# Optimization experiments

Hardware: AMD Instinct MI355X
Metric: run time of the kernel (lower is better)

## Reference

```python
import jax, jax.numpy as jnp
import numpy as np

B, T, D, U, O = 256, 1024, 256, 512, 256

def setup_inputs() -> dict:
    key = jax.random.key(0)
    kx, kk, kr, kd = jax.random.split(key, 4)
    # he_normal-style scaling for weights
    x = jax.random.normal(kx, (B, T, D), dtype=jnp.float32)
    Wk = jax.random.normal(kk, (D, U), dtype=jnp.float32) * np.sqrt(2.0 / D)
    Wr = jax.random.normal(kr, (U, U), dtype=jnp.float32) * np.sqrt(2.0 / U)
    Wd = jax.random.normal(kd, (U, O), dtype=jnp.float32) * np.sqrt(2.0 / U)
    h0 = jnp.zeros((B, U), dtype=jnp.float32)  # stateful RNN initial state
    return {"x": x, "Wk": Wk, "Wr": Wr, "Wd": Wd, "h0": h0}

def reference(x, Wk, Wr, Wd, h0):
    # SimpleRNN (no bias): h_t = tanh(x_t @ Wk + h_{t-1} @ Wr)
    # return_sequences=False -> only final hidden state; then Dense (no bias).
    # Precompute the input projection for all timesteps in one big GEMM.
    xp = jnp.einsum('btd,du->btu', x, Wk)           # [B, T, U]
    xs = jnp.swapaxes(xp, 0, 1)                     # [T, B, U] for scan

    def step(h, xt):
        h = jnp.tanh(xt + h @ Wr)
        return h, None

    hT, _ = jax.lax.scan(step, h0, xs)              # hT: [B, U]
    return hT @ Wd                                  # [B, O]
```

## Files before the change

kernel.cpp:

```cpp
#include <hip/hip_runtime.h>
#include <hip/hip_bf16.h>

#define T_STEPS 1024
#define B_SZ 256
#define D_SZ 256
#define U_SZ 512
#define O_SZ 256
#define K_TOT 768

#define ROWS_PER_WG 16
#define COLS_PER_WG 32
#define GROUPS 16
#define COLGRPS 16
#define WAVES_PER_GROUP 32
#define WT_PITCH 776
#define CTR_PITCH 1056

typedef __attribute__((ext_vector_type(8))) short short8;
typedef __attribute__((ext_vector_type(4))) float floatx4;
typedef __attribute__((ext_vector_type(4))) int int4v;
typedef __attribute__((ext_vector_type(4))) unsigned int uint4v;

__device__ __forceinline__ unsigned short f2bf(float f) {
  union { float f; unsigned int u; } v; v.f = f;
  unsigned int r = v.u + 0x7FFFu + ((v.u >> 16) & 1u);
  return (unsigned short)(r >> 16);
}
__device__ __forceinline__ float bf2f(unsigned short s) {
  union { unsigned int u; float f; } v; v.u = ((unsigned int)s) << 16;
  return v.f;
}
__device__ __forceinline__ unsigned int pk2(float a, float b) {
  union { __hip_bfloat162 h; unsigned int u; } cv;
  cv.h = __float22bfloat162_rn(make_float2(a, b));
  return cv.u;
}

__device__ __forceinline__ void store_short_l3(const unsigned short* p, unsigned int v) {
  asm volatile("global_store_short %0, %1, off sc0 sc1"
               :: "v"(p), "v"(v) : "memory");
}
__device__ __forceinline__ int4v load16_l3(const unsigned short* p) {
  int4v r;
  asm volatile("global_load_dwordx4 %0, %1, off sc0 sc1"
               : "=v"(r) : "v"(p) : "memory");
  return r;
}
__device__ __forceinline__ void wait_vm0() {
  asm volatile("s_waitcnt vmcnt(0)" ::: "memory");
}
__device__ __forceinline__ unsigned int load_ctr_l3(const unsigned int* p) {
  unsigned int r;
  asm volatile("global_load_dword %0, %1, off sc0 sc1\n\ts_waitcnt vmcnt(0)"
               : "=v"(r) : "v"(p) : "memory");
  return r;
}

extern "C" __global__ void __launch_bounds__(128)
rnn_persistent(const float* __restrict__ x, const float* __restrict__ Wk,
               const float* __restrict__ Wr, const float* __restrict__ h0,
               unsigned short* __restrict__ Hbuf0, unsigned short* __restrict__ Hbuf1,
               unsigned int* __restrict__ ctr)
{
  __shared__ unsigned short Wt[COLS_PER_WG][WT_PITCH];

  const int bid  = blockIdx.x;
  const int g    = (bid & 7) + ((bid >> 7) << 3);
  const int c    = (bid >> 3) & 15;
  const int row0 = g * ROWS_PER_WG;
  const int col0 = c * COLS_PER_WG;
  const int tid  = threadIdx.x;
  const int wave = tid >> 6;
  const int lane = tid & 63;
  const int m    = lane & 15;
  const int quad = lane >> 4;
  unsigned int* gctr = ctr + g * CTR_PITCH;

  for (int idx = tid; idx < COLS_PER_WG * K_TOT; idx += 128) {
    int k  = idx >> 5;
    int cl = idx & 31;
    float w = (k < D_SZ) ? Wk[(size_t)k * U_SZ + col0 + cl]
                         : Wr[(size_t)(k - D_SZ) * U_SZ + col0 + cl];
    Wt[cl][k] = f2bf(w);
  }

  {
    int e  = tid * 4;
    int rr = e >> 5;
    int cl = e & 31;
    const float* src = h0 + (size_t)(row0 + rr) * U_SZ + col0 + cl;
    const unsigned short* dst = Hbuf0 + (size_t)(row0 + rr) * U_SZ + col0 + cl;
    store_short_l3(dst + 0, f2bf(src[0]));
    store_short_l3(dst + 1, f2bf(src[1]));
    store_short_l3(dst + 2, f2bf(src[2]));
    store_short_l3(dst + 3, f2bf(src[3]));
  }
  wait_vm0();
  __syncthreads();
  if (lane == 0)
    __hip_atomic_fetch_add(gctr, 1u, __ATOMIC_RELAXED, __HIP_MEMORY_SCOPE_AGENT);

  const int n_l = (wave << 4) + m;
  const unsigned short* wrow = &Wt[n_l][0];
  const float* xrow = x + (size_t)(row0 + m) * T_STEPS * D_SZ + quad * 8;
  const int colg = col0 + n_l;

  const unsigned short* bufs[2] = { Hbuf0, Hbuf1 };

  for (int t = 0; t < T_STEPS; ++t) {
    floatx4 acc = {0.f, 0.f, 0.f, 0.f};

    const float* xp = xrow + (size_t)t * D_SZ;
#pragma unroll
    for (int kb = 0; kb < 8; ++kb) {
      floatx4 lo = *(const floatx4*)(xp + kb * 32);
      floatx4 hi = *(const floatx4*)(xp + kb * 32 + 4);
      union { short8 s; uint4v u; } fu;
      fu.u[0] = pk2(lo[0], lo[1]); fu.u[1] = pk2(lo[2], lo[3]);
      fu.u[2] = pk2(hi[0], hi[1]); fu.u[3] = pk2(hi[2], hi[3]);
      short8 bf = *(const short8*)(wrow + kb * 32 + quad * 8);
      acc = __builtin_amdgcn_mfma_f32_16x16x32_bf16(fu.s, bf, acc, 0, 0, 0);
    }

    {
      const unsigned int* cp = gctr + t;
      for (;;) {
        unsigned int cnt = load_ctr_l3(cp);
        if (cnt >= WAVES_PER_GROUP) break;
        __builtin_amdgcn_s_sleep(1);
      }
    }

    const unsigned short* Hr = bufs[t & 1] + (size_t)(row0 + m) * U_SZ + quad * 8;
    int4v araw[16];
#pragma unroll
    for (int kb = 0; kb < 16; ++kb)
      araw[kb] = load16_l3(Hr + kb * 32);
    wait_vm0();
#pragma unroll
    for (int kb = 0; kb < 16; ++kb) {
      union { int4v i; short8 s; } uc; uc.i = araw[kb];
      short8 bf = *(const short8*)(wrow + D_SZ + kb * 32 + quad * 8);
      acc = __builtin_amdgcn_mfma_f32_16x16x32_bf16(uc.s, bf, acc, 0, 0, 0);
    }

    const unsigned short* Hw = bufs[(t + 1) & 1];
#pragma unroll
    for (int i = 0; i < 4; ++i) {
      float v = tanhf(acc[i]);
      store_short_l3(Hw + (size_t)(row0 + quad * 4 + i) * U_SZ + colg, f2bf(v));
    }
    wait_vm0();
    if (lane == 0)
      __hip_atomic_fetch_add(gctr + t + 1, 1u, __ATOMIC_RELAXED, __HIP_MEMORY_SCOPE_AGENT);
  }
}

extern "C" __global__ void __launch_bounds__(256)
out_gemm(const unsigned short* __restrict__ Hf, const float* __restrict__ Wd,
         float* __restrict__ out)
{
  int b = blockIdx.x;
  int o = threadIdx.x;
  const unsigned short* hrow = Hf + (size_t)b * U_SZ;
  float acc = 0.f;
#pragma unroll 8
  for (int k = 0; k < U_SZ; ++k)
    acc += bf2f(hrow[k]) * Wd[(size_t)k * O_SZ + o];
  out[(size_t)b * O_SZ + o] = acc;
}

extern "C" void kernel_launch(void* const* d_in, const int* in_sizes, int n_in,
                              void* d_out, int out_size, void* d_ws, size_t ws_size,
                              hipStream_t stream)
{
  const float* x  = (const float*)d_in[0];
  const float* Wk = (const float*)d_in[1];
  const float* Wr = (const float*)d_in[2];
  const float* Wd = (const float*)d_in[3];
  const float* h0 = (const float*)d_in[4];
  float* out = (float*)d_out;

  unsigned short* H0 = (unsigned short*)d_ws;
  unsigned short* H1 = H0 + (size_t)B_SZ * U_SZ;
  unsigned int*  ctr = (unsigned int*)((char*)d_ws + (size_t)2 * B_SZ * U_SZ * 2);

  hipMemsetAsync(ctr, 0, (size_t)GROUPS * CTR_PITCH * sizeof(unsigned int), stream);

  void* args[] = { (void*)&x, (void*)&Wk, (void*)&Wr, (void*)&h0,
                   (void*)&H0, (void*)&H1, (void*)&ctr };
  hipLaunchCooperativeKernel((void*)rnn_persistent, dim3(GROUPS * COLGRPS),
                             dim3(128), args, 0, stream);

  out_gemm<<<dim3(B_SZ), dim3(O_SZ), 0, stream>>>(H0, Wd, out);
}
```

Baseline: 4.657 ms.

## Pin row groups to one XCD and use XCD-local cache scope for recurrence

```diff
diff --git a/kernel.cpp b/kernel.cpp
--- a/kernel.cpp
+++ b/kernel.cpp
@@ -12,9 +12,10 @@
 #define COLS_PER_WG 32
 #define GROUPS 16
 #define COLGRPS 16
-#define WAVES_PER_GROUP 32
-#define WT_PITCH 776
+#define NUM_WGS 256
 #define CTR_PITCH 1056
+#define GRID_SLOT (GROUPS * CTR_PITCH)
+#define MISM_SLOT (GRID_SLOT + 1)
 
 typedef __attribute__((ext_vector_type(8))) short short8;
 typedef __attribute__((ext_vector_type(4))) float floatx4;
@@ -35,25 +36,98 @@
   cv.h = __float22bfloat162_rn(make_float2(a, b));
   return cv.u;
 }
-
-__device__ __forceinline__ void store_short_l3(const unsigned short* p, unsigned int v) {
-  asm volatile("global_store_short %0, %1, off sc0 sc1"
-               :: "v"(p), "v"(v) : "memory");
-}
-__device__ __forceinline__ int4v load16_l3(const unsigned short* p) {
-  int4v r;
-  asm volatile("global_load_dwordx4 %0, %1, off sc0 sc1"
-               : "=v"(r) : "v"(p) : "memory");
-  return r;
-}
 __device__ __forceinline__ void wait_vm0() {
   asm volatile("s_waitcnt vmcnt(0)" ::: "memory");
 }
-__device__ __forceinline__ unsigned int load_ctr_l3(const unsigned int* p) {
+
+template <bool FAST>
+__device__ __forceinline__ void store_h(const unsigned short* p, unsigned int v) {
+  if constexpr (FAST)
+    asm volatile("global_store_short %0, %1, off" :: "v"(p), "v"(v) : "memory");
+  else
+    asm volatile("global_store_short %0, %1, off sc0 sc1" :: "v"(p), "v"(v) : "memory");
+}
+template <bool FAST>
+__device__ __forceinline__ int4v load16(const unsigned short* p) {
+  int4v r;
+  if constexpr (FAST)
+    asm volatile("global_load_dwordx4 %0, %1, off sc0" : "=v"(r) : "v"(p) : "memory");
+  else
+    asm volatile("global_load_dwordx4 %0, %1, off sc0 sc1" : "=v"(r) : "v"(p) : "memory");
+  return r;
+}
+template <bool FAST>
+__device__ __forceinline__ unsigned int load_ctr(const unsigned int* p) {
   unsigned int r;
-  asm volatile("global_load_dword %0, %1, off sc0 sc1\n\ts_waitcnt vmcnt(0)"
-               : "=v"(r) : "v"(p) : "memory");
+  if constexpr (FAST)
+    asm volatile("global_load_dword %0, %1, off sc0\n\ts_waitcnt vmcnt(0)"
+                 : "=v"(r) : "v"(p) : "memory");
+  else
+    asm volatile("global_load_dword %0, %1, off sc0 sc1\n\ts_waitcnt vmcnt(0)"
+                 : "=v"(r) : "v"(p) : "memory");
   return r;
+}
+template <bool FAST>
+__device__ __forceinline__ void arrive(unsigned int* p) {
+  if constexpr (FAST)
+    asm volatile("global_atomic_add %0, %1, off" :: "v"(p), "v"(1u) : "memory");
+  else
+    __hip_atomic_fetch_add(p, 1u, __ATOMIC_RELAXED, __HIP_MEMORY_SCOPE_AGENT);
+}
+
+template <bool FAST>
+__device__ __forceinline__ void run_loop(const float* xrow, const unsigned short* wq,
+                                         const unsigned short* Hb0, const unsigned short* Hb1,
+                                         unsigned int* gctr, int row0, int colg,
+                                         int m, int quad, int tid)
+{
+  const unsigned short* bufs[2] = { Hb0, Hb1 };
+  for (int t = 0; t < T_STEPS; ++t) {
+    floatx4 acc = {0.f, 0.f, 0.f, 0.f};
+
+    const float* xp = xrow + (size_t)t * D_SZ;
+#pragma unroll
+    for (int kb = 0; kb < 8; ++kb) {
+      floatx4 lo = *(const floatx4*)(xp + kb * 32);
+      floatx4 hi = *(const floatx4*)(xp + kb * 32 + 4);
+      union { short8 s; uint4v u; } fu;
+      fu.u[0] = pk2(lo[0], lo[1]); fu.u[1] = pk2(lo[2], lo[3]);
+      fu.u[2] = pk2(hi[0], hi[1]); fu.u[3] = pk2(hi[2], hi[3]);
+      short8 bfr = *(const short8*)(wq + kb * 1024);
+      acc = __builtin_amdgcn_mfma_f32_16x16x32_bf16(fu.s, bfr, acc, 0, 0, 0);
+    }
+
+    {
+      const unsigned int* cp = gctr + t;
+      for (;;) {
+        if (load_ctr<FAST>(cp) >= COLGRPS) break;
+        __builtin_amdgcn_s_sleep(1);
+      }
+    }
+
+    const unsigned short* Hr = bufs[t & 1] + (size_t)(row0 + m) * U_SZ + quad * 8;
+    int4v araw[16];
+#pragma unroll
+    for (int kb = 0; kb < 16; ++kb)
+      araw[kb] = load16<FAST>(Hr + kb * 32);
+    wait_vm0();
+#pragma unroll
+    for (int kb = 0; kb < 16; ++kb) {
+      union { int4v i; short8 s; } uc; uc.i = araw[kb];
+      short8 bfr = *(const short8*)(wq + (kb + 8) * 1024);
+      acc = __builtin_amdgcn_mfma_f32_16x16x32_bf16(uc.s, bfr, acc, 0, 0, 0);
+    }
+
+    const unsigned short* Hw = bufs[(t + 1) & 1];
+#pragma unroll
+    for (int i = 0; i < 4; ++i) {
+      float v = tanhf(acc[i]);
+      store_h<FAST>(Hw + (size_t)(row0 + quad * 4 + i) * U_SZ + colg, f2bf(v));
+    }
+    wait_vm0();
+    __syncthreads();
+    if (tid == 0) arrive<FAST>(gctr + t + 1);
+  }
 }
 
 extern "C" __global__ void __launch_bounds__(128)
@@ -62,10 +136,10 @@
                unsigned short* __restrict__ Hbuf0, unsigned short* __restrict__ Hbuf1,
                unsigned int* __restrict__ ctr)
 {
-  __shared__ unsigned short Wt[COLS_PER_WG][WT_PITCH];
+  __shared__ unsigned short Wt[K_TOT * COLS_PER_WG];
 
   const int bid  = blockIdx.x;
-  const int g    = (bid & 7) + ((bid >> 7) << 3);
+  const int g    = (bid & 7) * 2 + (bid >> 7);
   const int c    = (bid >> 3) & 15;
   const int row0 = g * ROWS_PER_WG;
   const int col0 = c * COLS_PER_WG;
@@ -81,8 +155,25 @@
     int cl = idx & 31;
     float w = (k < D_SZ) ? Wk[(size_t)k * U_SZ + col0 + cl]
                          : Wr[(size_t)(k - D_SZ) * U_SZ + col0 + cl];
-    Wt[cl][k] = f2bf(w);
-  }
+    int off = (((k >> 5) * 4 + ((k >> 3) & 3)) * 32 + cl) * 8 + (k & 7);
+    Wt[off] = f2bf(w);
+  }
+
+  unsigned int xcc;
+  asm volatile("s_getreg_b32 %0, hwreg(HW_REG_XCC_ID)" : "=s"(xcc));
+  xcc &= 0xF;
+  if (tid == 0 && xcc != (unsigned int)(bid & 7))
+    __hip_atomic_fetch_or(ctr + MISM_SLOT, 1u, __ATOMIC_RELAXED, __HIP_MEMORY_SCOPE_AGENT);
+  wait_vm0();
+  __syncthreads();
+  if (tid == 0)
+    __hip_atomic_fetch_add(ctr + GRID_SLOT, 1u, __ATOMIC_RELAXED, __HIP_MEMORY_SCOPE_AGENT);
+  if (tid == 0) {
+    while (load_ctr<false>(ctr + GRID_SLOT) < NUM_WGS)
+      __builtin_amdgcn_s_sleep(4);
+  }
+  __syncthreads();
+  const bool fast = (load_ctr<false>(ctr + MISM_SLOT) == 0);
 
   {
     int e  = tid * 4;
@@ -90,70 +181,30 @@
     int cl = e & 31;
     const float* src = h0 + (size_t)(row0 + rr) * U_SZ + col0 + cl;
     const unsigned short* dst = Hbuf0 + (size_t)(row0 + rr) * U_SZ + col0 + cl;
-    store_short_l3(dst + 0, f2bf(src[0]));
-    store_short_l3(dst + 1, f2bf(src[1]));
-    store_short_l3(dst + 2, f2bf(src[2]));
-    store_short_l3(dst + 3, f2bf(src[3]));
+    if (fast) {
+      store_h<true>(dst + 0, f2bf(src[0])); store_h<true>(dst + 1, f2bf(src[1]));
+      store_h<true>(dst + 2, f2bf(src[2])); store_h<true>(dst + 3, f2bf(src[3]));
+    } else {
+      store_h<false>(dst + 0, f2bf(src[0])); store_h<false>(dst + 1, f2bf(src[1]));
+      store_h<false>(dst + 2, f2bf(src[2])); store_h<false>(dst + 3, f2bf(src[3]));
+    }
   }
   wait_vm0();
   __syncthreads();
-  if (lane == 0)
-    __hip_atomic_fetch_add(gctr, 1u, __ATOMIC_RELAXED, __HIP_MEMORY_SCOPE_AGENT);
-
-  const int n_l = (wave << 4) + m;
-  const unsigned short* wrow = &Wt[n_l][0];
+  if (tid == 0) {
+    if (fast) arrive<true>(gctr);
+    else      arrive<false>(gctr);
+  }
+
+  const int n_l  = (wave << 4) + m;
+  const int colg = col0 + n_l;
+  const unsigned short* wq = &Wt[quad * 256 + n_l * 8];
   const float* xrow = x + (size_t)(row0 + m) * T_STEPS * D_SZ + quad * 8;
-  const int colg = col0 + n_l;
-
-  const unsigned short* bufs[2] = { Hbuf0, Hbuf1 };
-
-  for (int t = 0; t < T_STEPS; ++t) {
-    floatx4 acc = {0.f, 0.f, 0.f, 0.f};
-
-    const float* xp = xrow + (size_t)t * D_SZ;
-#pragma unroll
-    for (int kb = 0; kb < 8; ++kb) {
-      floatx4 lo = *(const floatx4*)(xp + kb * 32);
-      floatx4 hi = *(const floatx4*)(xp + kb * 32 + 4);
-      union { short8 s; uint4v u; } fu;
-      fu.u[0] = pk2(lo[0], lo[1]); fu.u[1] = pk2(lo[2], lo[3]);
-      fu.u[2] = pk2(hi[0], hi[1]); fu.u[3] = pk2(hi[2], hi[3]);
-      short8 bf = *(const short8*)(wrow + kb * 32 + quad * 8);
-      acc = __builtin_amdgcn_mfma_f32_16x16x32_bf16(fu.s, bf, acc, 0, 0, 0);
-    }
-
-    {
-      const unsigned int* cp = gctr + t;
-      for (;;) {
-        unsigned int cnt = load_ctr_l3(cp);
-        if (cnt >= WAVES_PER_GROUP) break;
-        __builtin_amdgcn_s_sleep(1);
-      }
-    }
-
-    const unsigned short* Hr = bufs[t & 1] + (size_t)(row0 + m) * U_SZ + quad * 8;
-    int4v araw[16];
-#pragma unroll
-    for (int kb = 0; kb < 16; ++kb)
-      araw[kb] = load16_l3(Hr + kb * 32);
-    wait_vm0();
-#pragma unroll
-    for (int kb = 0; kb < 16; ++kb) {
-      union { int4v i; short8 s; } uc; uc.i = araw[kb];
-      short8 bf = *(const short8*)(wrow + D_SZ + kb * 32 + quad * 8);
-      acc = __builtin_amdgcn_mfma_f32_16x16x32_bf16(uc.s, bf, acc, 0, 0, 0);
-    }
-
-    const unsigned short* Hw = bufs[(t + 1) & 1];
-#pragma unroll
-    for (int i = 0; i < 4; ++i) {
-      float v = tanhf(acc[i]);
-      store_short_l3(Hw + (size_t)(row0 + quad * 4 + i) * U_SZ + colg, f2bf(v));
-    }
-    wait_vm0();
-    if (lane == 0)
-      __hip_atomic_fetch_add(gctr + t + 1, 1u, __ATOMIC_RELAXED, __HIP_MEMORY_SCOPE_AGENT);
-  }
+
+  if (fast)
+    run_loop<true>(xrow, wq, Hbuf0, Hbuf1, gctr, row0, colg, m, quad, tid);
+  else
+    run_loop<false>(xrow, wq, Hbuf0, Hbuf1, gctr, row0, colg, m, quad, tid);
 }
 
 extern "C" __global__ void __launch_bounds__(256)
@@ -185,11 +236,11 @@
   unsigned short* H1 = H0 + (size_t)B_SZ * U_SZ;
   unsigned int*  ctr = (unsigned int*)((char*)d_ws + (size_t)2 * B_SZ * U_SZ * 2);
 
-  hipMemsetAsync(ctr, 0, (size_t)GROUPS * CTR_PITCH * sizeof(unsigned int), stream);
+  hipMemsetAsync(ctr, 0, (size_t)(GROUPS * CTR_PITCH + 64) * sizeof(unsigned int), stream);
 
   void* args[] = { (void*)&x, (void*)&Wk, (void*)&Wr, (void*)&h0,
                    (void*)&H0, (void*)&H1, (void*)&ctr };
-  hipLaunchCooperativeKernel((void*)rnn_persistent, dim3(GROUPS * COLGRPS),
+  hipLaunchCooperativeKernel((void*)rnn_persistent, dim3(NUM_WGS),
                              dim3(128), args, 0, stream);
 
   out_gemm<<<dim3(B_SZ), dim3(O_SZ), 0, stream>>>(H0, Wd, out);
```

Measured after the change: 3.861 ms. -17.1%, faster.
